# Optimization experiments

Hardware: AMD Instinct MI355X
Metric: run time of the kernel (lower is better)

Reference implementation:

```python
import jax, jax.numpy as jnp
import numpy as np

D_MODEL = 1024
N_HEAD = 16
D_K = 64
D_V = 64
LN_EPS = 1e-5


def setup_inputs() -> dict:
    key = jax.random.key(0)
    ks = jax.random.split(key, 12)
    B, S = 4, 2048
    s = 1.0 / np.sqrt(D_MODEL)
    inp = {
        "q": jax.random.normal(ks[0], (B, S, D_MODEL), jnp.float32),
        "k": jax.random.normal(ks[1], (B, S, D_MODEL), jnp.float32),
        "v": jax.random.normal(ks[2], (B, S, D_MODEL), jnp.float32),
        "mask": jnp.ones((B, S, S), jnp.int32),
        "w_q": jax.random.normal(ks[3], (D_MODEL, N_HEAD * D_K), jnp.float32) * s,
        "b_q": jnp.zeros((N_HEAD * D_K,), jnp.float32),
        "w_k": jax.random.normal(ks[4], (D_MODEL, N_HEAD * D_K), jnp.float32) * s,
        "b_k": jnp.zeros((N_HEAD * D_K,), jnp.float32),
        "w_v": jax.random.normal(ks[5], (D_MODEL, N_HEAD * D_V), jnp.float32) * s,
        "b_v": jnp.zeros((N_HEAD * D_V,), jnp.float32),
        "w_fc": jax.random.normal(ks[6], (N_HEAD * D_V, D_MODEL), jnp.float32) * s,
        "b_fc": jnp.zeros((D_MODEL,), jnp.float32),
        "ln_g": jnp.ones((D_MODEL,), jnp.float32),
        "ln_b": jnp.zeros((D_MODEL,), jnp.float32),
    }
    return inp


def reference(q, k, v, mask, w_q, b_q, w_k, b_k, w_v, b_v, w_fc, b_fc, ln_g, ln_b):
    B, Sq, _ = q.shape
    Sk = k.shape[1]
    residual = q
    # QKV projections -> [B, H, S, d]
    qh = (q @ w_q + b_q).reshape(B, Sq, N_HEAD, D_K).transpose(0, 2, 1, 3)
    kh = (k @ w_k + b_k).reshape(B, Sk, N_HEAD, D_K).transpose(0, 2, 1, 3)
    vh = (v @ w_v + b_v).reshape(B, Sk, N_HEAD, D_V).transpose(0, 2, 1, 3)
    temp = jnp.sqrt(jnp.asarray(D_K, qh.dtype))
    scores = jnp.einsum("bhqd,bhkd->bhqk", qh / temp, kh)
    scores = jnp.where(mask[:, None, :, :] == 0, jnp.asarray(-1e9, scores.dtype), scores)
    attn = jax.nn.softmax(scores, axis=-1)  # dropout is identity in eval
    out = jnp.einsum("bhqk,bhkd->bhqd", attn, vh)
    out = out.transpose(0, 2, 1, 3).reshape(B, Sq, N_HEAD * D_V)
    out = out @ w_fc + b_fc  # output proj (dropout identity)
    x = out + residual
    mu = jnp.mean(x, axis=-1, keepdims=True)
    var = jnp.mean(jnp.square(x - mu), axis=-1, keepdims=True)
    y = (x - mu) * jax.lax.rsqrt(var + LN_EPS) * ln_g + ln_b
    return (y, attn)
```

## Files before the change

### kernel.cpp

```cpp
#include <hip/hip_runtime.h>
#include <cstdint>
#include <cstddef>

#define DM 1024
#define HN 16
#define DH 64
#define BB 4
#define SS 2048
#define MM (BB * SS)

typedef __bf16 bf16;
typedef bf16 bf16x8 __attribute__((ext_vector_type(8)));
typedef bf16 bf16x4 __attribute__((ext_vector_type(4)));
typedef float f32x4 __attribute__((ext_vector_type(4)));
typedef int i32x4 __attribute__((ext_vector_type(4)));

__device__ __forceinline__ f32x4 mfma16(bf16x8 a, bf16x8 b, f32x4 c) {
  return __builtin_amdgcn_mfma_f32_16x16x32_bf16(a, b, c, 0, 0, 0);
}

typedef __attribute__((address_space(3))) void lds_void_t;
typedef __attribute__((address_space(1))) void glob_void_t;

__device__ __forceinline__ void gload16(const void* g, void* l) {
  __builtin_amdgcn_global_load_lds((const glob_void_t*)g, (lds_void_t*)l, 16, 0, 0);
}

__global__ __launch_bounds__(256) void mask_bitsT(const int* __restrict__ mask,
                                                  unsigned int* __restrict__ mT) {
  int qt = blockIdx.x, b = blockIdx.y;
  int col0 = threadIdx.x * 8;
  unsigned int m[8] = {0, 0, 0, 0, 0, 0, 0, 0};
  const int* mp = mask + ((size_t)b * SS + qt * 32) * SS + col0;
  for (int r = 0; r < 32; ++r) {
    i32x4 a = *(const i32x4*)(mp + (size_t)r * SS);
    i32x4 c = *(const i32x4*)(mp + (size_t)r * SS + 4);
#pragma unroll
    for (int i = 0; i < 4; ++i) {
      m[i] |= (unsigned int)(a[i] != 0) << r;
      m[4 + i] |= (unsigned int)(c[i] != 0) << r;
    }
  }
#pragma unroll
  for (int i = 0; i < 8; ++i)
    mT[((size_t)b * 64 + qt) * SS + col0 + i] = m[i];
}

__global__ __launch_bounds__(256) void cvt3(const float* __restrict__ q,
                                            const float* __restrict__ k,
                                            const float* __restrict__ v,
                                            bf16* __restrict__ dst) {
  int which = blockIdx.y;
  const float* in = which == 0 ? q : which == 1 ? k : v;
  bf16* out = dst + (size_t)which * MM * DM;
  int i = (blockIdx.x * 256 + threadIdx.x) * 8;
  f32x4 a = *(const f32x4*)(in + i);
  f32x4 b = *(const f32x4*)(in + i + 4);
  bf16x8 o;
  o[0] = (bf16)a[0]; o[1] = (bf16)a[1]; o[2] = (bf16)a[2]; o[3] = (bf16)a[3];
  o[4] = (bf16)b[0]; o[5] = (bf16)b[1]; o[6] = (bf16)b[2]; o[7] = (bf16)b[3];
  *(bf16x8*)(out + i) = o;
}

__global__ __launch_bounds__(256) void wtrans4(const float* __restrict__ w_q,
                                               const float* __restrict__ w_k,
                                               const float* __restrict__ w_v,
                                               const float* __restrict__ w_fc,
                                               bf16* __restrict__ WT) {
  int p = blockIdx.z;
  const float* W = p == 0 ? w_q : p == 1 ? w_k : p == 2 ? w_v : w_fc;
  bf16* out = WT + (size_t)p * DM * DM;
  __shared__ float t[32][33];
  int n0 = blockIdx.x * 32, k0 = blockIdx.y * 32;
  int tid = threadIdx.x;
  int r = tid >> 3, c = (tid & 7) * 4;
  f32x4 v = *(const f32x4*)&W[(size_t)(k0 + r) * DM + n0 + c];
  t[r][c] = v[0]; t[r][c + 1] = v[1]; t[r][c + 2] = v[2]; t[r][c + 3] = v[3];
  __syncthreads();
  bf16x4 o;
#pragma unroll
  for (int i = 0; i < 4; ++i) o[i] = (bf16)t[c + i][r];
  *(bf16x4*)&out[(size_t)(n0 + r) * DM + k0 + c] = o;
}

__global__ __launch_bounds__(256) void gemm_qkv(const bf16* __restrict__ Abase,
                                                const bf16* __restrict__ Bt,
                                                const float* __restrict__ b_q,
                                                const float* __restrict__ b_k,
                                                const float* __restrict__ b_v,
                                                bf16* __restrict__ qhh,
                                                bf16* __restrict__ khh,
                                                bf16* __restrict__ vhT) {
  constexpr int K = DM;
  __shared__ bf16 Ab[128 * 32];
  __shared__ bf16 Bb[128 * 32];
  int tid = threadIdx.x, wave = tid >> 6, lane = tid & 63;
  int bm = blockIdx.x * 128, bn = blockIdx.y * 128;
  int proj = bn >> 10;
  const bf16* A = Abase + (size_t)proj * MM * DM;
  const float* bias = proj == 0 ? b_q : proj == 1 ? b_k : b_v;
  int wr = (wave >> 1) * 64, wc = (wave & 1) * 64;
  int fr = lane & 15, kg8 = (lane >> 4) * 8;
  f32x4 acc[4][4] = {};
  int arow = tid >> 2, acol = (tid & 3) * 8;
  const bf16* Ag0 = A + (size_t)(bm + arow) * K + acol;
  const bf16* Ag1 = Ag0 + (size_t)64 * K;
  const bf16* Bg0 = Bt + (size_t)(bn + arow) * K + acol;
  const bf16* Bg1 = Bg0 + (size_t)64 * K;
  char* la = (char*)Ab + wave * 1024;
  char* lb = (char*)Bb + wave * 1024;
  for (int k0 = 0; k0 < K; k0 += 32) {
    __syncthreads();
    gload16(Ag0 + k0, la);
    gload16(Ag1 + k0, la + 4096);
    gload16(Bg0 + k0, lb);
    gload16(Bg1 + k0, lb + 4096);
    asm volatile("s_waitcnt vmcnt(0)" ::: "memory");
    __syncthreads();
    bf16x8 af[4], bfr[4];
#pragma unroll
    for (int m = 0; m < 4; ++m)
      af[m] = *(const bf16x8*)&Ab[(wr + m * 16 + fr) * 32 + kg8];
#pragma unroll
    for (int n = 0; n < 4; ++n)
      bfr[n] = *(const bf16x8*)&Bb[(wc + n * 16 + fr) * 32 + kg8];
#pragma unroll
    for (int m = 0; m < 4; ++m)
#pragma unroll
      for (int n = 0; n < 4; ++n) acc[m][n] = mfma16(af[m], bfr[n], acc[m][n]);
  }
  int b = bm >> 11;
#pragma unroll
  for (int m = 0; m < 4; ++m)
#pragma unroll
    for (int n = 0; n < 4; ++n) {
      int c = bn + wc + n * 16 + fr;
      int lc = c & 1023;
      float bv = bias[lc];
      int h = lc >> 6, d = lc & 63;
      int r0 = bm + wr + m * 16 + (lane >> 4) * 4;
      int s0 = r0 & (SS - 1);
      if (proj == 2) {
        bf16x4 o;
#pragma unroll
        for (int j = 0; j < 4; ++j) o[j] = (bf16)(acc[m][n][j] + bv);
        *(bf16x4*)&vhT[(size_t)(b * HN + h) * (SS * DH) +
                       (size_t)(s0 >> 5) * (DH * 32) + d * 32 + (s0 & 31)] = o;
      } else {
        bf16* dst = proj == 0 ? qhh : khh;
        float sc = proj == 0 ? 0.125f : 1.f;
#pragma unroll
        for (int j = 0; j < 4; ++j) {
          float v = (acc[m][n][j] + bv) * sc;
          dst[(size_t)(b * HN + h) * (SS * DH) + (size_t)(s0 + j) * DH + d] =
              (bf16)v;
        }
      }
    }
}

__global__ __launch_bounds__(256) void gemm_out(const bf16* __restrict__ A,
                                                const bf16* __restrict__ Bt,
                                                const float* __restrict__ bias,
                                                const float* __restrict__ resid,
                                                float* __restrict__ out) {
  constexpr int K = DM;
  __shared__ bf16 Ab[128 * 32];
  __shared__ bf16 Bb[128 * 32];
  int tid = threadIdx.x, wave = tid >> 6, lane = tid & 63;
  int bm = blockIdx.x * 128, bn = blockIdx.y * 128;
  int wr = (wave >> 1) * 64, wc = (wave & 1) * 64;
  int fr = lane & 15, kg8 = (lane >> 4) * 8;
  f32x4 acc[4][4] = {};
  int arow = tid >> 2, acol = (tid & 3) * 8;
  const bf16* Ag0 = A + (size_t)(bm + arow) * K + acol;
  const bf16* Ag1 = Ag0 + (size_t)64 * K;
  const bf16* Bg0 = Bt + (size_t)(bn + arow) * K + acol;
  const bf16* Bg1 = Bg0 + (size_t)64 * K;
  char* la = (char*)Ab + wave * 1024;
  char* lb = (char*)Bb + wave * 1024;
  for (int k0 = 0; k0 < K; k0 += 32) {
    __syncthreads();
    gload16(Ag0 + k0, la);
    gload16(Ag1 + k0, la + 4096);
    gload16(Bg0 + k0, lb);
    gload16(Bg1 + k0, lb + 4096);
    asm volatile("s_waitcnt vmcnt(0)" ::: "memory");
    __syncthreads();
    bf16x8 af[4], bfr[4];
#pragma unroll
    for (int m = 0; m < 4; ++m)
      af[m] = *(const bf16x8*)&Ab[(wr + m * 16 + fr) * 32 + kg8];
#pragma unroll
    for (int n = 0; n < 4; ++n)
      bfr[n] = *(const bf16x8*)&Bb[(wc + n * 16 + fr) * 32 + kg8];
#pragma unroll
    for (int m = 0; m < 4; ++m)
#pragma unroll
      for (int n = 0; n < 4; ++n) acc[m][n] = mfma16(af[m], bfr[n], acc[m][n]);
  }
#pragma unroll
  for (int m = 0; m < 4; ++m)
#pragma unroll
    for (int n = 0; n < 4; ++n) {
      int c = bn + wc + n * 16 + fr;
      float bv = bias[c];
#pragma unroll
      for (int j = 0; j < 4; ++j) {
        int r = bm + wr + m * 16 + (lane >> 4) * 4 + j;
        size_t idx = (size_t)r * DM + c;
        out[idx] = acc[m][n][j] + bv + resid[idx];
      }
    }
}

__global__ __launch_bounds__(1024, 4) void attn_kernel(
    const bf16* __restrict__ qh, const bf16* __restrict__ kh,
    const bf16* __restrict__ vhT, const unsigned int* __restrict__ mT,
    float* __restrict__ attn_out, bf16* __restrict__ ctx) {
  extern __shared__ char smem[];
  float* pbuf = (float*)(smem + 32 * 4096);
  float* invp = (float*)(smem + 32 * 4096 + 8192);
  int tid = threadIdx.x, wave = tid >> 6, lane = tid & 63;
  int fid = (blockIdx.x & 7) * 512 + (blockIdx.x >> 3);
  int bh = fid >> 6, qt = fid & 63;
  int b = bh >> 4, h = bh & 15;
  int q0 = qt * 32;
  const bf16* qbase = qh + ((size_t)bh * SS + q0) * DH;
  const bf16* kbase = kh + (size_t)bh * SS * DH;
  const bf16* vbase = vhT + (size_t)bh * SS * DH;
  const unsigned int* mTb = mT + ((size_t)b * 64 + qt) * SS;
  int fr = lane & 15, kg = lane >> 4;

  bf16x8 qa0 = *(const bf16x8*)&qbase[(size_t)fr * DH + kg * 8];
  bf16x8 qa1 = *(const bf16x8*)&qbase[(size_t)fr * DH + 32 + kg * 8];
  bf16x8 qb0 = *(const bf16x8*)&qbase[(size_t)(16 + fr) * DH + kg * 8];
  bf16x8 qb1 = *(const bf16x8*)&qbase[(size_t)(16 + fr) * DH + 32 + kg * 8];

  {
    int sw = wave * 128;
    bf16x8 kb0[8], kb1[8];
    auto kload = [&](int g) {
      const bf16* kp = kbase + (size_t)(sw + g * 16 + fr) * DH + kg * 8;
      kb0[g & 7] = *(const bf16x8*)kp;
      kb1[g & 7] = *(const bf16x8*)(kp + 32);
    };
#pragma unroll
    for (int g = 0; g < 4; ++g) kload(g);
#pragma unroll
    for (int g = 0; g < 8; ++g) {
      if (g < 4) kload(g + 4);
      f32x4 aa = {0.f, 0.f, 0.f, 0.f};
      f32x4 ab = {0.f, 0.f, 0.f, 0.f};
      aa = mfma16(qa0, kb0[g & 7], aa);
      aa = mfma16(qa1, kb1[g & 7], aa);
      ab = mfma16(qb0, kb0[g & 7], ab);
      ab = mfma16(qb1, kb1[g & 7], ab);
      int col = sw + g * 16 + fr;
      unsigned int bits = mTb[col];
      int slot = col >> 3, within = col & 7;
#pragma unroll
      for (int j = 0; j < 4; ++j) {
        int ra = kg * 4 + j;
        int rb = ra + 16;
        float fa = ((bits >> ra) & 1u) ? __expf(aa[j]) : 0.f;
        float fb = ((bits >> rb) & 1u) ? __expf(ab[j]) : 0.f;
        *(bf16*)(smem + ra * 4096 + ((slot ^ ra) << 4) + within * 2) = (bf16)fa;
        *(bf16*)(smem + rb * 4096 + ((slot ^ rb) << 4) + within * 2) = (bf16)fb;
      }
    }
  }
  __syncthreads();

  {
    int row = wave * 2 + (lane >> 5);
    int la = lane & 31;
    char* rbase = smem + row * 4096;
    float sum = 0.f;
#pragma unroll
    for (int it = 0; it < 8; ++it) {
      int slot = la + it * 32;
      bf16x8 e = *(const bf16x8*)(rbase + ((slot ^ row) << 4));
#pragma unroll
      for (int i = 0; i < 8; ++i) sum += (float)e[i];
    }
#pragma unroll
    for (int off = 1; off < 32; off <<= 1) sum += __shfl_xor(sum, off);
    if (la == 0) invp[row] = 1.f / sum;
  }
  __syncthreads();

  {
    int rb = wave >> 3, dq = (wave >> 1) & 3, kh2 = wave & 1;
    f32x4 cacc = {0.f, 0.f, 0.f, 0.f};
    const bf16* vtile = vbase + (size_t)(kh2 * 32) * (DH * 32) +
                        (dq * 16 + fr) * 32 + kg * 8;
    int prow_row = rb * 16 + fr;
    char* prow = smem + prow_row * 4096;
    bf16x8 vb[8], pb[8];
    auto pvload = [&](int kk) {
      vb[kk & 7] = *(const bf16x8*)&vtile[(size_t)kk * (DH * 32)];
      int slotA = kh2 * 128 + kk * 4 + kg;
      pb[kk & 7] = *(const bf16x8*)(prow + ((slotA ^ prow_row) << 4));
    };
    pvload(0);
    pvload(1);
    pvload(2);
    pvload(3);
#pragma unroll
    for (int kk = 0; kk < 32; ++kk) {
      if (kk < 28) pvload(kk + 4);
      cacc = mfma16(pb[kk & 7], vb[kk & 7], cacc);
    }
    if (kh2 == 1) {
#pragma unroll
      for (int j = 0; j < 4; ++j)
        pbuf[((rb * 4 + dq) * 16 + kg * 4 + j) * 16 + fr] = cacc[j];
    }
    __syncthreads();
    if (kh2 == 0) {
#pragma unroll
      for (int j = 0; j < 4; ++j) {
        int row = rb * 16 + kg * 4 + j;
        float v = (cacc[j] + pbuf[((rb * 4 + dq) * 16 + kg * 4 + j) * 16 + fr]) *
                  invp[row];
        ctx[((size_t)b * SS + q0 + row) * DM + h * DH + dq * 16 + fr] = (bf16)v;
      }
    }
  }

  {
    int t = tid & 511, rh = tid >> 9;
    int slot = t >> 1, halfoff = (t & 1) * 8;
    float* outb = attn_out + ((size_t)bh * SS + q0) * SS;
#pragma unroll
    for (int it = 0; it < 16; ++it) {
      int r = it * 2 + rh;
      bf16x4 e = *(const bf16x4*)(smem + r * 4096 + ((slot ^ r) << 4) + halfoff);
      float inv = invp[r];
      f32x4 u = {(float)e[0] * inv, (float)e[1] * inv, (float)e[2] * inv,
                 (float)e[3] * inv};
      *(f32x4*)(outb + (size_t)r * SS + t * 4) = u;
    }
  }
}

__global__ __launch_bounds__(256) void ln_k(float* __restrict__ x,
                                            const float* __restrict__ g,
                                            const float* __restrict__ bln) {
  int r = blockIdx.x, tid = threadIdx.x;
  f32x4 v = *(const f32x4*)&x[(size_t)r * DM + tid * 4];
  float s = v[0] + v[1] + v[2] + v[3];
  float s2 = v[0] * v[0] + v[1] * v[1] + v[2] * v[2] + v[3] * v[3];
#pragma unroll
  for (int off = 32; off; off >>= 1) {
    s += __shfl_down(s, off);
    s2 += __shfl_down(s2, off);
  }
  __shared__ float rs_[4], rs2_[4];
  int wave = tid >> 6, lane = tid & 63;
  if (lane == 0) {
    rs_[wave] = s;
    rs2_[wave] = s2;
  }
  __syncthreads();
  s = rs_[0] + rs_[1] + rs_[2] + rs_[3];
  s2 = rs2_[0] + rs2_[1] + rs2_[2] + rs2_[3];
  float mu = s * (1.f / DM);
  float var = s2 * (1.f / DM) - mu * mu;
  float rstd = rsqrtf(var + 1e-5f);
  f32x4 gg = *(const f32x4*)&g[tid * 4];
  f32x4 bb = *(const f32x4*)&bln[tid * 4];
  f32x4 o;
#pragma unroll
  for (int i = 0; i < 4; ++i) o[i] = (v[i] - mu) * rstd * gg[i] + bb[i];
  *(f32x4*)&x[(size_t)r * DM + tid * 4] = o;
}

extern "C" void kernel_launch(void* const* d_in, const int* in_sizes, int n_in,
                              void* d_out, int out_size, void* d_ws,
                              size_t ws_size, hipStream_t stream) {
  const float* q = (const float*)d_in[0];
  const float* k = (const float*)d_in[1];
  const float* v = (const float*)d_in[2];
  const int* mask = (const int*)d_in[3];
  const float* w_q = (const float*)d_in[4];
  const float* b_q = (const float*)d_in[5];
  const float* w_k = (const float*)d_in[6];
  const float* b_k = (const float*)d_in[7];
  const float* w_v = (const float*)d_in[8];
  const float* b_v = (const float*)d_in[9];
  const float* w_fc = (const float*)d_in[10];
  const float* b_fc = (const float*)d_in[11];
  const float* ln_g = (const float*)d_in[12];
  const float* ln_b = (const float*)d_in[13];

  float* y = (float*)d_out;
  float* attn_out = (float*)d_out + (size_t)MM * DM;

  char* w = (char*)d_ws;
  const size_t actN = (size_t)MM * DM;
  bf16* qkv_bf = (bf16*)w;  w += 3 * actN * 2;
  bf16* wT = (bf16*)w;      w += (size_t)4 * DM * DM * 2;
  bf16* qhh = (bf16*)w;     w += actN * 2;
  bf16* khh = (bf16*)w;     w += actN * 2;
  bf16* vhT = (bf16*)w;     w += actN * 2;
  bf16* ctx = (bf16*)w;     w += actN * 2;
  unsigned int* mT = (unsigned int*)w;  w += (size_t)BB * 64 * SS * 4;

  mask_bitsT<<<dim3(SS / 32, BB), 256, 0, stream>>>(mask, mT);
  cvt3<<<dim3(4096, 3), 256, 0, stream>>>(q, k, v, qkv_bf);
  wtrans4<<<dim3(DM / 32, DM / 32, 4), 256, 0, stream>>>(w_q, w_k, w_v, w_fc, wT);
  gemm_qkv<<<dim3(MM / 128, 3072 / 128), 256, 0, stream>>>(
      qkv_bf, wT, b_q, b_k, b_v, qhh, khh, vhT);
  hipFuncSetAttribute((const void*)attn_kernel,
                      hipFuncAttributeMaxDynamicSharedMemorySize, 139392);
  attn_kernel<<<4096, 1024, 139392, stream>>>(
      qhh, khh, vhT, mT, attn_out, ctx);
  gemm_out<<<dim3(MM / 128, DM / 128), 256, 0, stream>>>(
      ctx, wT + (size_t)3 * DM * DM, b_fc, q, y);
  ln_k<<<MM, 256, 0, stream>>>(y, ln_g, ln_b);
}
```

Baseline: 667.2 us.

## Fuse row sums into exp pass and interleave attn stores with PV MFMAs

Row sums of the exponentiated scores are now built in registers during the QK pass, reduced with shuffles, and combined across waves through a small LDS buffer. This replaces the separate pass that reread the whole 32x2048 bf16 probability tile from LDS. The fp32 attention-probability writeback to global memory is moved inside the PV MFMA loop so the stores overlap with the matrix work, instead of running as a tail phase. The sums now come from fp32 values rather than bf16-rounded ones, so the normalization differs slightly, and LDS use grows a little.

```diff
diff --git a/kernel.cpp b/kernel.cpp
--- a/kernel.cpp
+++ b/kernel.cpp
@@ -219,8 +219,9 @@
     const bf16* __restrict__ vhT, const unsigned int* __restrict__ mT,
     float* __restrict__ attn_out, bf16* __restrict__ ctx) {
   extern __shared__ char smem[];
-  float* pbuf = (float*)(smem + 32 * 4096);
-  float* invp = (float*)(smem + 32 * 4096 + 8192);
+  float* wsum = (float*)(smem + 131072);
+  float* invp = (float*)(smem + 131072 + 2048);
+  float* pbuf = (float*)(smem + 131072 + 2048 + 128);
   int tid = threadIdx.x, wave = tid >> 6, lane = tid & 63;
   int fid = (blockIdx.x & 7) * 512 + (blockIdx.x >> 3);
   int bh = fid >> 6, qt = fid & 63;
@@ -237,6 +238,7 @@
   bf16x8 qb0 = *(const bf16x8*)&qbase[(size_t)(16 + fr) * DH + kg * 8];
   bf16x8 qb1 = *(const bf16x8*)&qbase[(size_t)(16 + fr) * DH + 32 + kg * 8];
 
+  float rs[8] = {0.f, 0.f, 0.f, 0.f, 0.f, 0.f, 0.f, 0.f};
   {
     int sw = wave * 128;
     bf16x8 kb0[8], kb1[8];
@@ -265,28 +267,31 @@
         int rb = ra + 16;
         float fa = ((bits >> ra) & 1u) ? __expf(aa[j]) : 0.f;
         float fb = ((bits >> rb) & 1u) ? __expf(ab[j]) : 0.f;
+        rs[j] += fa;
+        rs[4 + j] += fb;
         *(bf16*)(smem + ra * 4096 + ((slot ^ ra) << 4) + within * 2) = (bf16)fa;
         *(bf16*)(smem + rb * 4096 + ((slot ^ rb) << 4) + within * 2) = (bf16)fb;
       }
     }
   }
+#pragma unroll
+  for (int j = 0; j < 8; ++j) {
+#pragma unroll
+    for (int off = 1; off < 16; off <<= 1) rs[j] += __shfl_xor(rs[j], off);
+  }
+  if (fr == 0) {
+#pragma unroll
+    for (int j = 0; j < 4; ++j) {
+      wsum[wave * 32 + kg * 4 + j] = rs[j];
+      wsum[wave * 32 + 16 + kg * 4 + j] = rs[4 + j];
+    }
+  }
   __syncthreads();
-
-  {
-    int row = wave * 2 + (lane >> 5);
-    int la = lane & 31;
-    char* rbase = smem + row * 4096;
-    float sum = 0.f;
-#pragma unroll
-    for (int it = 0; it < 8; ++it) {
-      int slot = la + it * 32;
-      bf16x8 e = *(const bf16x8*)(rbase + ((slot ^ row) << 4));
-#pragma unroll
-      for (int i = 0; i < 8; ++i) sum += (float)e[i];
-    }
-#pragma unroll
-    for (int off = 1; off < 32; off <<= 1) sum += __shfl_xor(sum, off);
-    if (la == 0) invp[row] = 1.f / sum;
+  if (tid < 32) {
+    float s = 0.f;
+#pragma unroll
+    for (int w = 0; w < 16; ++w) s += wsum[w * 32 + tid];
+    invp[tid] = 1.f / s;
   }
   __syncthreads();
 
@@ -297,6 +302,9 @@
                         (dq * 16 + fr) * 32 + kg * 8;
     int prow_row = rb * 16 + fr;
     char* prow = smem + prow_row * 4096;
+    int srow0 = 2 * wave, srow1 = 2 * wave + 1;
+    float inv0 = invp[srow0], inv1 = invp[srow1];
+    float* outb = attn_out + ((size_t)bh * SS + q0) * SS;
     bf16x8 vb[8], pb[8];
     auto pvload = [&](int kk) {
       vb[kk & 7] = *(const bf16x8*)&vtile[(size_t)kk * (DH * 32)];
@@ -311,6 +319,18 @@
     for (int kk = 0; kk < 32; ++kk) {
       if (kk < 28) pvload(kk + 4);
       cacc = mfma16(pb[kk & 7], vb[kk & 7], cacc);
+      if ((kk & 1) == 0) {
+        int i = kk >> 1;
+        int row = (i & 1) ? srow1 : srow0;
+        float inv = (i & 1) ? inv1 : inv0;
+        int col0 = (i >> 1) * 256 + lane * 4;
+        int slot = col0 >> 3;
+        bf16x4 e = *(const bf16x4*)(smem + row * 4096 + ((slot ^ row) << 4) +
+                                    (col0 & 7) * 2);
+        f32x4 u = {(float)e[0] * inv, (float)e[1] * inv, (float)e[2] * inv,
+                   (float)e[3] * inv};
+        *(f32x4*)(outb + (size_t)row * SS + col0) = u;
+      }
     }
     if (kh2 == 1) {
 #pragma unroll
@@ -326,21 +346,6 @@
                   invp[row];
         ctx[((size_t)b * SS + q0 + row) * DM + h * DH + dq * 16 + fr] = (bf16)v;
       }
-    }
-  }
-
-  {
-    int t = tid & 511, rh = tid >> 9;
-    int slot = t >> 1, halfoff = (t & 1) * 8;
-    float* outb = attn_out + ((size_t)bh * SS + q0) * SS;
-#pragma unroll
-    for (int it = 0; it < 16; ++it) {
-      int r = it * 2 + rh;
-      bf16x4 e = *(const bf16x4*)(smem + r * 4096 + ((slot ^ r) << 4) + halfoff);
-      float inv = invp[r];
-      f32x4 u = {(float)e[0] * inv, (float)e[1] * inv, (float)e[2] * inv,
-                 (float)e[3] * inv};
-      *(f32x4*)(outb + (size_t)r * SS + t * 4) = u;
     }
   }
 }
@@ -414,8 +419,8 @@
   gemm_qkv<<<dim3(MM / 128, 3072 / 128), 256, 0, stream>>>(
       qkv_bf, wT, b_q, b_k, b_v, qhh, khh, vhT);
   hipFuncSetAttribute((const void*)attn_kernel,
-                      hipFuncAttributeMaxDynamicSharedMemorySize, 139392);
-  attn_kernel<<<4096, 1024, 139392, stream>>>(
+                      hipFuncAttributeMaxDynamicSharedMemorySize, 141440);
+  attn_kernel<<<4096, 1024, 141440, stream>>>(
       qhh, khh, vhT, mT, attn_out, ctx);
   gemm_out<<<dim3(MM / 128, DM / 128), 256, 0, stream>>>(
       ctx, wT + (size_t)3 * DM * DM, b_fc, q, y);
```

Result: slower. 743.8 us (+11.5%).

## Specialize waves: half do full-K PV MFMA, half stream attention writes

Applied to the files above, without the earlier changes.

Splits the 16 waves of the attention block so waves 0-7 compute the full 64-step PV product without a K-split, and waves 8-15 concurrently write the normalized fp32 attention matrix to global memory. This removes the cross-wave partial-sum buffer, its extra barrier, and 8 KB of LDS, and raises MFMA wave priority with s_setprio. In exchange each PV wave runs a serial chain twice as long, and the attention store is done by half as many threads.

```diff
diff --git a/kernel.cpp b/kernel.cpp
--- a/kernel.cpp
+++ b/kernel.cpp
@@ -219,8 +219,7 @@
     const bf16* __restrict__ vhT, const unsigned int* __restrict__ mT,
     float* __restrict__ attn_out, bf16* __restrict__ ctx) {
   extern __shared__ char smem[];
-  float* pbuf = (float*)(smem + 32 * 4096);
-  float* invp = (float*)(smem + 32 * 4096 + 8192);
+  float* invp = (float*)(smem + 32 * 4096);
   int tid = threadIdx.x, wave = tid >> 6, lane = tid & 63;
   int fid = (blockIdx.x & 7) * 512 + (blockIdx.x >> 3);
   int bh = fid >> 6, qt = fid & 63;
@@ -262,11 +261,11 @@
 #pragma unroll
       for (int j = 0; j < 4; ++j) {
         int ra = kg * 4 + j;
-        int rb = ra + 16;
+        int rb_ = ra + 16;
         float fa = ((bits >> ra) & 1u) ? __expf(aa[j]) : 0.f;
-        float fb = ((bits >> rb) & 1u) ? __expf(ab[j]) : 0.f;
+        float fb = ((bits >> rb_) & 1u) ? __expf(ab[j]) : 0.f;
         *(bf16*)(smem + ra * 4096 + ((slot ^ ra) << 4) + within * 2) = (bf16)fa;
-        *(bf16*)(smem + rb * 4096 + ((slot ^ rb) << 4) + within * 2) = (bf16)fb;
+        *(bf16*)(smem + rb_ * 4096 + ((slot ^ rb_) << 4) + within * 2) = (bf16)fb;
       }
     }
   }
@@ -290,52 +289,41 @@
   }
   __syncthreads();
 
-  {
-    int rb = wave >> 3, dq = (wave >> 1) & 3, kh2 = wave & 1;
+  if (wave < 8) {
+    int rb = wave >> 2, dq = wave & 3;
     f32x4 cacc = {0.f, 0.f, 0.f, 0.f};
-    const bf16* vtile = vbase + (size_t)(kh2 * 32) * (DH * 32) +
-                        (dq * 16 + fr) * 32 + kg * 8;
+    const bf16* vtile = vbase + (dq * 16 + fr) * 32 + kg * 8;
     int prow_row = rb * 16 + fr;
     char* prow = smem + prow_row * 4096;
     bf16x8 vb[8], pb[8];
     auto pvload = [&](int kk) {
       vb[kk & 7] = *(const bf16x8*)&vtile[(size_t)kk * (DH * 32)];
-      int slotA = kh2 * 128 + kk * 4 + kg;
+      int slotA = kk * 4 + kg;
       pb[kk & 7] = *(const bf16x8*)(prow + ((slotA ^ prow_row) << 4));
     };
     pvload(0);
     pvload(1);
     pvload(2);
     pvload(3);
-#pragma unroll
-    for (int kk = 0; kk < 32; ++kk) {
-      if (kk < 28) pvload(kk + 4);
+    __builtin_amdgcn_s_setprio(1);
+#pragma unroll
+    for (int kk = 0; kk < 64; ++kk) {
+      if (kk < 60) pvload(kk + 4);
       cacc = mfma16(pb[kk & 7], vb[kk & 7], cacc);
     }
-    if (kh2 == 1) {
-#pragma unroll
-      for (int j = 0; j < 4; ++j)
-        pbuf[((rb * 4 + dq) * 16 + kg * 4 + j) * 16 + fr] = cacc[j];
-    }
-    __syncthreads();
-    if (kh2 == 0) {
-#pragma unroll
-      for (int j = 0; j < 4; ++j) {
-        int row = rb * 16 + kg * 4 + j;
-        float v = (cacc[j] + pbuf[((rb * 4 + dq) * 16 + kg * 4 + j) * 16 + fr]) *
-                  invp[row];
-        ctx[((size_t)b * SS + q0 + row) * DM + h * DH + dq * 16 + fr] = (bf16)v;
-      }
-    }
-  }
-
-  {
-    int t = tid & 511, rh = tid >> 9;
+    __builtin_amdgcn_s_setprio(0);
+#pragma unroll
+    for (int j = 0; j < 4; ++j) {
+      int row = rb * 16 + kg * 4 + j;
+      float v = cacc[j] * invp[row];
+      ctx[((size_t)b * SS + q0 + row) * DM + h * DH + dq * 16 + fr] = (bf16)v;
+    }
+  } else {
+    int t = (wave - 8) * 64 + lane;
     int slot = t >> 1, halfoff = (t & 1) * 8;
     float* outb = attn_out + ((size_t)bh * SS + q0) * SS;
-#pragma unroll
-    for (int it = 0; it < 16; ++it) {
-      int r = it * 2 + rh;
+#pragma unroll 4
+    for (int r = 0; r < 32; ++r) {
       bf16x4 e = *(const bf16x4*)(smem + r * 4096 + ((slot ^ r) << 4) + halfoff);
       float inv = invp[r];
       f32x4 u = {(float)e[0] * inv, (float)e[1] * inv, (float)e[2] * inv,
@@ -414,8 +402,8 @@
   gemm_qkv<<<dim3(MM / 128, 3072 / 128), 256, 0, stream>>>(
       qkv_bf, wT, b_q, b_k, b_v, qhh, khh, vhT);
   hipFuncSetAttribute((const void*)attn_kernel,
-                      hipFuncAttributeMaxDynamicSharedMemorySize, 139392);
-  attn_kernel<<<4096, 1024, 139392, stream>>>(
+                      hipFuncAttributeMaxDynamicSharedMemorySize, 131200);
+  attn_kernel<<<4096, 1024, 131200, stream>>>(
       qhh, khh, vhT, mT, attn_out, ctx);
   gemm_out<<<dim3(MM / 128, DM / 128), 256, 0, stream>>>(
       ctx, wT + (size_t)3 * DM * DM, b_fc, q, y);
```

New measurement: 645.1 us (median of 2 runs). -3.3%, faster.
